# Performance work log

Hardware: AMD Instinct MI355X
Metric: run time of the kernel (lower is better)

The kernel has to match this reference:

```python
import jax, jax.numpy as jnp
import numpy as np

N = 4096        # number of nodes
C = 512         # in_features
L_LAT = 64      # L_latent
EPS = 0.25      # epsilon


def setup_inputs() -> dict:
    key = jax.random.key(0)
    ks = jax.random.split(key, 8)
    def lin(k, fan_in, shape):
        return (jax.random.normal(k, shape, jnp.float32) / np.float32(np.sqrt(fan_in)))
    x = jax.random.normal(ks[0], (N, C), jnp.float32)
    adj = jax.random.uniform(ks[1], (N, N), jnp.float32)  # dense nonneg kernel
    W_proj = lin(ks[2], C, (C, L_LAT)); b_proj = jnp.zeros((L_LAT,), jnp.float32)
    W_pi1 = lin(ks[3], L_LAT, (L_LAT, C)); b_pi1 = jnp.zeros((C,), jnp.float32)
    W_pi2 = lin(ks[4], C, (C, 1)); b_pi2 = jnp.zeros((1,), jnp.float32)
    W_f = lin(ks[5], C, (C, C)); b_f = jnp.zeros((C,), jnp.float32)
    dt = jnp.array([0.1], jnp.float32)
    return {"x": x, "adj": adj, "W_proj": W_proj, "b_proj": b_proj,
            "W_pi1": W_pi1, "b_pi1": b_pi1, "W_pi2": W_pi2, "b_pi2": b_pi2,
            "W_f": W_f, "b_f": b_f, "dt": dt}


def reference(x, adj, W_proj, b_proj, W_pi1, b_pi1, W_pi2, b_pi2, W_f, b_f, dt):
    # proj_list: x -> latent [n, L]
    z = x @ W_proj + b_proj
    # pi_list: Linear -> ReLU -> Linear -> Sigmoid, squeeze to [n]
    pi = jax.nn.sigmoid(jax.nn.relu(z @ W_pi1 + b_pi1) @ W_pi2 + b_pi2)[:, 0]
    # q_epsilon_tilde: row sums of the kernel
    q = adj.sum(axis=1)                       # [n]
    # K_tilde = K_epsilon @ diag(pi/q)  == column scaling
    K_tilde = adj * (pi / q)[None, :]         # [n, n]
    # D_tilde diagonal; torch.inverse of a diagonal == elementwise reciprocal
    d = K_tilde.sum(axis=1) + 1e-5            # [n]
    # target = relu(f(x)) with f = Linear(C, C)
    target = jax.nn.relu(x @ W_f + b_f)       # [n, C]
    # L @ target = (1/eps) * diag(1/d) @ K_tilde @ target - target
    Lt = (K_tilde @ target) / (EPS * d)[:, None] - target
    return target + dt[0] * Lt
```

## Files before the change

### kernel.cpp

```cpp
#include <hip/hip_runtime.h>
#include <hip/hip_bf16.h>

#define N_NODES 4096
#define C_DIM   512
#define L_DIM   64
#define SPLITS  4
#define KCHUNK  (N_NODES / SPLITS)

typedef unsigned short u16;
typedef unsigned int   u32;
using bf16x8 = __attribute__((ext_vector_type(8))) __bf16;
using u16x8  = __attribute__((ext_vector_type(8))) unsigned short;
using f32x4  = __attribute__((ext_vector_type(4))) float;

__device__ __forceinline__ float b2f(u16 u) {
    union { unsigned int i; float f; } v; v.i = ((unsigned int)u) << 16; return v.f;
}
__device__ __forceinline__ u16 f2b(float f) {
    unsigned int u = __float_as_uint(f);
    u += 0x7fff + ((u >> 16) & 1);
    return (u16)(u >> 16);
}
__device__ __forceinline__ void gload16(const void* g, void* l) {
    __builtin_amdgcn_global_load_lds((const __attribute__((address_space(1))) void*)g,
                                     (__attribute__((address_space(3))) void*)l,
                                     16, 0, 0);
}
__device__ __forceinline__ int detect_mode_inl(const u16* __restrict__ adj) {
    int m = 0;
#pragma unroll
    for (int i = 0; i < 64; ++i) m |= (adj[i] >= 0x8000) ? 1 : 0;
    return m;
}

#define OFF_MODE  0
#define OFF_DT    64
#define OFF_BIAS  1024
#define OFF_BP    4096
#define OFF_BP1   4608
#define OFF_WP2   8192
#define OFF_BP2   10240
#define OFF_Q     16384
#define OFF_S     32768
#define OFF_DV    49152
#define OFF_WPP   65536
#define OFF_WP1P  131072
#define OFF_WFT   196608
#define OFF_T     1048576
#define OFF_TST   9437184
#define OFF_XB    13631488
#define OFF_ADJB  17825792

__device__ __forceinline__ float ldin(const void* p, int i, int mode) {
    if (mode) return ((const float*)p)[i];
    return b2f(((const u16*)p)[i]);
}

__global__ __launch_bounds__(256) void k1_prep(const void* __restrict__ adj, const void* __restrict__ x,
        const void* Wp, const void* bp, const void* Wp1, const void* bp1,
        const void* Wp2, const void* bp2, const void* Wf, const void* bfc, const void* dt,
        int* __restrict__ modep,
        float* __restrict__ bp_f, float* __restrict__ bp1_f,
        float* __restrict__ Wp2_f, float* __restrict__ bp2_f,
        float* __restrict__ bias_f, float* __restrict__ dt_f,
        u32* __restrict__ WpP, u32* __restrict__ Wp1P,
        u16* __restrict__ adjb, float* __restrict__ q, u16* __restrict__ xb,
        u16* __restrict__ WfT) {
    __shared__ float tile[32][33];
    int bid = blockIdx.x, tid = threadIdx.x;
    int mode = detect_mode_inl((const u16*)adj);
    if (bid < 7) {
        if (bid == 0 && tid == 0) *modep = mode;
        int idx = bid * 256 + tid;
        if (idx < 64)           bp_f[idx]          = ldin(bp,  idx, mode);
        else if (idx < 576)     bp1_f[idx - 64]    = ldin(bp1, idx - 64, mode);
        else if (idx < 1088)    Wp2_f[idx - 576]   = ldin(Wp2, idx - 576, mode);
        else if (idx == 1088)   bp2_f[0]           = ldin(bp2, 0, mode);
        else if (idx < 1601)    bias_f[idx - 1089] = ldin(bfc, idx - 1089, mode);
        else if (idx == 1601)   dt_f[0]            = ldin(dt, 0, mode);
    } else if (bid < 2055) {
        if (mode == 0) return;
        int idx = (bid - 7) * 256 + tid;
        float4 v = ((const float4*)x)[idx];
        ushort4 o; o.x = f2b(v.x); o.y = f2b(v.y); o.z = f2b(v.z); o.w = f2b(v.w);
        ((ushort4*)xb)[idx] = o;
    } else if (bid < 3079) {
        int wave = tid >> 6, lane = tid & 63;
        int row = (bid - 2055) * 4 + wave;
        float acc = 0.f;
        if (mode) {
            const float4* rp = (const float4*)((const float*)adj + (size_t)row * N_NODES);
            ushort4* wp = (ushort4*)(adjb + (size_t)row * N_NODES);
#pragma unroll
            for (int it = 0; it < 16; ++it) {
                float4 v = rp[it * 64 + lane];
                acc += v.x + v.y + v.z + v.w;
                ushort4 o; o.x = f2b(v.x); o.y = f2b(v.y); o.z = f2b(v.z); o.w = f2b(v.w);
                wp[it * 64 + lane] = o;
            }
        } else {
            const u16x8* rp = (const u16x8*)((const u16*)adj + (size_t)row * N_NODES);
#pragma unroll
            for (int it = 0; it < 8; ++it) {
                u16x8 v = rp[it * 64 + lane];
#pragma unroll
                for (int e = 0; e < 8; ++e) acc += b2f(v[e]);
            }
        }
#pragma unroll
        for (int off = 32; off > 0; off >>= 1) acc += __shfl_down(acc, off);
        if (lane == 0) q[row] = acc;
    } else if (bid < 3335) {
        int g = bid - 3079;
        int tx = tid & 31, ty = tid >> 5;
        int x0 = (g & 15) * 32, y0 = (g >> 4) * 32;
        if (mode) {
            const float* src = (const float*)Wf;
#pragma unroll
            for (int r = ty; r < 32; r += 8) tile[r][tx] = src[(size_t)(y0 + r) * C_DIM + x0 + tx];
        } else {
            const u16* src = (const u16*)Wf;
#pragma unroll
            for (int r = ty; r < 32; r += 8) tile[r][tx] = b2f(src[(size_t)(y0 + r) * C_DIM + x0 + tx]);
        }
        __syncthreads();
#pragma unroll
        for (int r = ty; r < 32; r += 8)
            WfT[(size_t)(x0 + r) * C_DIM + y0 + tx] = f2b(tile[tx][r]);
    } else if (bid < 3399) {
        int idx = (bid - 3335) * 256 + tid;
        int k2i = idx >> 6, j = idx & 63;
        float a = ldin(Wp, (2 * k2i) * L_DIM + j, mode);
        float b = ldin(Wp, (2 * k2i + 1) * L_DIM + j, mode);
        WpP[idx] = (u32)f2b(a) | ((u32)f2b(b) << 16);
    } else {
        int idx = (bid - 3399) * 256 + tid;
        int jj2 = idx >> 9, m = idx & 511;
        float a = ldin(Wp1, (2 * jj2) * C_DIM + m, mode);
        float b = ldin(Wp1, (2 * jj2 + 1) * C_DIM + m, mode);
        Wp1P[idx] = (u32)f2b(a) | ((u32)f2b(b) << 16);
    }
}

__global__ __launch_bounds__(256) void k2_pi_gemm1(const void* __restrict__ xraw,
        const int* __restrict__ modep, const u16* __restrict__ xb, const u16* __restrict__ WfT,
        const u32* __restrict__ WpP, const u32* __restrict__ Wp1P,
        const float* __restrict__ bp_f,  const float* __restrict__ bp1_f,
        const float* __restrict__ Wp2_f, const float* __restrict__ bp2_f,
        const float* __restrict__ bias_f, const float* __restrict__ dt_f,
        const float* __restrict__ q, float* __restrict__ s, float* __restrict__ T,
        void* __restrict__ out, float* __restrict__ Pacc) {
    __shared__ __align__(16) char smem[26880];
    int bid = blockIdx.x, tid = threadIdx.x;
    int mode = *modep;
    if (bid < 512) {
        float (*sx)[C_DIM]      = (float(*)[C_DIM])smem;
        float (*red)[8][L_DIM]  = (float(*)[8][L_DIM])(smem + 16384);
        float (*sz)[L_DIM]      = (float(*)[L_DIM])(smem + 24576);
        float (*rw)[8]          = (float(*)[8])(smem + 26624);
        int i0 = bid * 8;
        const u16* xsrc = mode ? xb : (const u16*)xraw;
        const u16x8* xp = (const u16x8*)(xsrc + (size_t)i0 * C_DIM);
#pragma unroll
        for (int r = 0; r < 2; ++r) {
            u16x8 v = xp[tid + 256 * r];
            float* dstf = &sx[0][0] + (size_t)(tid + 256 * r) * 8;
#pragma unroll
            for (int e = 0; e < 8; ++e) dstf[e] = b2f(v[e]);
        }
        __syncthreads();
        int j = tid & 63, part = tid >> 6;
        float za[8];
#pragma unroll
        for (int n = 0; n < 8; ++n) za[n] = 0.f;
        const u32* wp = WpP + part * 4096 + j;
#pragma unroll 8
        for (int kk = 0; kk < 64; ++kk) {
            u32 w = wp[kk * 64];
            float wa = b2f((u16)(w & 0xFFFF)), wb = b2f((u16)(w >> 16));
            int k = part * 128 + kk * 2;
#pragma unroll
            for (int n = 0; n < 8; ++n) za[n] += sx[n][k] * wa + sx[n][k + 1] * wb;
        }
#pragma unroll
        for (int n = 0; n < 8; ++n) red[part][n][j] = za[n];
        __syncthreads();
#pragma unroll
        for (int r = 0; r < 2; ++r) {
            int idx = tid + r * 256; int n = idx >> 6, jj = idx & 63;
            sz[n][jj] = red[0][n][jj] + red[1][n][jj] + red[2][n][jj] + red[3][n][jj] + bp_f[jj];
        }
        __syncthreads();
        int m0 = tid, m1 = tid + 256;
        float h0[8], h1[8];
        float b0 = bp1_f[m0], b1 = bp1_f[m1];
#pragma unroll
        for (int n = 0; n < 8; ++n) { h0[n] = b0; h1[n] = b1; }
        const u32* w1p = Wp1P + m0;
#pragma unroll 4
        for (int jj2 = 0; jj2 < 32; ++jj2) {
            u32 w0 = w1p[jj2 * 512], w1 = w1p[jj2 * 512 + 256];
            float w0a = b2f((u16)(w0 & 0xFFFF)), w0b = b2f((u16)(w0 >> 16));
            float w1a = b2f((u16)(w1 & 0xFFFF)), w1b = b2f((u16)(w1 >> 16));
#pragma unroll
            for (int n = 0; n < 8; ++n) {
                float za_ = sz[n][2 * jj2], zb_ = sz[n][2 * jj2 + 1];
                h0[n] += za_ * w0a + zb_ * w0b;
                h1[n] += za_ * w1a + zb_ * w1b;
            }
        }
        float w2a = Wp2_f[m0], w2b = Wp2_f[m1];
        float p[8];
#pragma unroll
        for (int n = 0; n < 8; ++n)
            p[n] = fmaxf(h0[n], 0.f) * w2a + fmaxf(h1[n], 0.f) * w2b;
#pragma unroll
        for (int off = 32; off > 0; off >>= 1)
#pragma unroll
            for (int n = 0; n < 8; ++n) p[n] += __shfl_down(p[n], off);
        int lane = tid & 63, wave = tid >> 6;
        if (lane == 0) {
#pragma unroll
            for (int n = 0; n < 8; ++n) rw[wave][n] = p[n];
        }
        __syncthreads();
        if (tid < 8) {
            float tot = rw[0][tid] + rw[1][tid] + rw[2][tid] + rw[3][tid] + bp2_f[0];
            float pi = 1.f / (1.f + expf(-tot));
            s[i0 + tid] = pi / q[i0 + tid];
        }
    } else {
        u16* lA = (u16*)smem;
        u16* lB = (u16*)(smem + 4096);
        const u16* A = mode ? xb : (const u16*)xraw;
        float* tgt = mode ? (float*)out : Pacc;
        int g = bid - 512;
        int lane = tid & 63, wave = tid >> 6;
        int bm = (g & 63) * 64, bn = (g >> 6) * 64;
        int quad = lane >> 4, l15 = lane & 15;
        int wm = wave * 16;
        const u16* Ap = A + (size_t)(bm + (tid >> 2)) * C_DIM + (tid & 3) * 8;
        const u16* Bp = WfT + (size_t)(bn + (tid >> 2)) * C_DIM + (tid & 3) * 8;
        u16* la = lA + tid * 8;
        u16* lb = lB + tid * 8;
        f32x4 acc[4];
#pragma unroll
        for (int nt = 0; nt < 4; ++nt) acc[nt] = (f32x4){0.f, 0.f, 0.f, 0.f};
        for (int k0 = 0; k0 < C_DIM; k0 += 32) {
            gload16(Ap + k0, la);
            gload16(Bp + k0, lb);
            __syncthreads();
            bf16x8 af = *(const bf16x8*)&lA[(wm + l15) * 32 + quad * 8];
            bf16x8 bfv[4];
#pragma unroll
            for (int nt = 0; nt < 4; ++nt) bfv[nt] = *(const bf16x8*)&lB[(nt * 16 + l15) * 32 + quad * 8];
#pragma unroll
            for (int nt = 0; nt < 4; ++nt)
                acc[nt] = __builtin_amdgcn_mfma_f32_16x16x32_bf16(af, bfv[nt], acc[nt], 0, 0, 0);
            __syncthreads();
        }
        float c0 = 1.f - dt_f[0];
#pragma unroll
        for (int nt = 0; nt < 4; ++nt) {
            int col = bn + nt * 16 + l15;
            float bv = bias_f[col];
#pragma unroll
            for (int r = 0; r < 4; ++r) {
                int row = bm + wm + quad * 4 + r;
                float t = fmaxf(acc[nt][r] + bv, 0.f);
                T[(size_t)row * C_DIM + col] = t;
                tgt[(size_t)row * C_DIM + col] = c0 * t;
            }
        }
    }
}

__global__ __launch_bounds__(256) void k3_mid(const void* __restrict__ adjraw,
        const int* __restrict__ modep,
        const u16* __restrict__ adjb, const float* __restrict__ s,
        const float* __restrict__ T,
        float* __restrict__ dv, u16* __restrict__ TsT) {
    __shared__ float tile[32][33];
    int bid = blockIdx.x, tid = threadIdx.x;
    int mode = *modep;
    if (bid < 1024) {
        const u16* A = mode ? adjb : (const u16*)adjraw;
        int wave = tid >> 6, lane = tid & 63;
        int row = bid * 4 + wave;
        const u16x8* rp = (const u16x8*)(A + (size_t)row * N_NODES);
        float acc = 0.f;
#pragma unroll
        for (int it = 0; it < 8; ++it) {
            int chunk = it * 64 + lane;
            u16x8 v = rp[chunk];
            const float4* sp = (const float4*)(s + chunk * 8);
            float4 s0 = sp[0], s1 = sp[1];
            acc += b2f(v[0]) * s0.x + b2f(v[1]) * s0.y + b2f(v[2]) * s0.z + b2f(v[3]) * s0.w;
            acc += b2f(v[4]) * s1.x + b2f(v[5]) * s1.y + b2f(v[6]) * s1.z + b2f(v[7]) * s1.w;
        }
#pragma unroll
        for (int off = 32; off > 0; off >>= 1) acc += __shfl_down(acc, off);
        if (lane == 0) dv[row] = acc + 1e-5f;
    } else {
        int g = bid - 1024;
        int tx = tid & 31, ty = tid >> 5;
        int x0 = (g & 15) * 32, y0 = (g >> 4) * 32;
#pragma unroll
        for (int r = ty; r < 32; r += 8) tile[r][tx] = T[(size_t)(y0 + r) * C_DIM + x0 + tx];
        __syncthreads();
        float sv = s[y0 + tx];
#pragma unroll
        for (int r = ty; r < 32; r += 8)
            TsT[(size_t)(x0 + r) * N_NODES + y0 + tx] = f2b(tile[tx][r] * sv);
    }
}

__global__ __launch_bounds__(256) void k4_gemm2(const void* __restrict__ adjraw,
        const int* __restrict__ modep,
        const u16* __restrict__ adjb, const u16* __restrict__ TsT,
        const float* __restrict__ dv, const float* __restrict__ dt_f,
        void* __restrict__ out, float* __restrict__ Pacc) {
    __shared__ __align__(16) u16 lA[8192];
    __shared__ __align__(16) u16 lB[8192];
    int mode = *modep;
    const u16* A = mode ? adjb : (const u16*)adjraw;
    float* tgt = mode ? (float*)out : Pacc;
    int tid = threadIdx.x;
    int lane = tid & 63, wave = tid >> 6;
    int bm = blockIdx.x * 128, bn = blockIdx.y * 128;
    int kbase = blockIdx.z * KCHUNK;
    int wm = (wave & 1) * 64, wn = (wave >> 1) * 64;
    int quad = lane >> 4, l15 = lane & 15;

    const u16* Ab0 = A + (size_t)(bm + (tid >> 2)) * N_NODES + kbase + (tid & 3) * 8;
    const u16* Ab1 = A + (size_t)(bm + 64 + (tid >> 2)) * N_NODES + kbase + (tid & 3) * 8;
    const u16* Bb0 = TsT + (size_t)(bn + (tid >> 2)) * N_NODES + kbase + (tid & 3) * 8;
    const u16* Bb1 = TsT + (size_t)(bn + 64 + (tid >> 2)) * N_NODES + kbase + (tid & 3) * 8;
    u16* la00 = lA + tid * 8;        u16* la01 = lA + 2048 + tid * 8;
    u16* la10 = lA + 4096 + tid * 8; u16* la11 = lA + 6144 + tid * 8;
    u16* lb00 = lB + tid * 8;        u16* lb01 = lB + 2048 + tid * 8;
    u16* lb10 = lB + 4096 + tid * 8; u16* lb11 = lB + 6144 + tid * 8;

    f32x4 acc[4][4];
#pragma unroll
    for (int a = 0; a < 4; ++a)
#pragma unroll
        for (int b = 0; b < 4; ++b) acc[a][b] = (f32x4){0.f, 0.f, 0.f, 0.f};

    for (int k0 = 0; k0 < KCHUNK; k0 += 64) {
        gload16(Ab0 + k0, la00);
        gload16(Ab1 + k0, la01);
        gload16(Ab0 + k0 + 32, la10);
        gload16(Ab1 + k0 + 32, la11);
        gload16(Bb0 + k0, lb00);
        gload16(Bb1 + k0, lb01);
        gload16(Bb0 + k0 + 32, lb10);
        gload16(Bb1 + k0 + 32, lb11);
        __syncthreads();
#pragma unroll
        for (int kk = 0; kk < 2; ++kk) {
            const u16* baseA = lA + kk * 4096;
            const u16* baseB = lB + kk * 4096;
            bf16x8 af[4], bfv[4];
#pragma unroll
            for (int mt = 0; mt < 4; ++mt) af[mt] = *(const bf16x8*)&baseA[(wm + mt * 16 + l15) * 32 + quad * 8];
#pragma unroll
            for (int nt = 0; nt < 4; ++nt) bfv[nt] = *(const bf16x8*)&baseB[(wn + nt * 16 + l15) * 32 + quad * 8];
#pragma unroll
            for (int mt = 0; mt < 4; ++mt)
#pragma unroll
                for (int nt = 0; nt < 4; ++nt)
                    acc[mt][nt] = __builtin_amdgcn_mfma_f32_16x16x32_bf16(af[mt], bfv[nt], acc[mt][nt], 0, 0, 0);
        }
        __syncthreads();
    }

    float c1 = dt_f[0] * 4.f;
#pragma unroll
    for (int mt = 0; mt < 4; ++mt) {
        float inv[4];
#pragma unroll
        for (int r = 0; r < 4; ++r) inv[r] = c1 / dv[bm + wm + mt * 16 + quad * 4 + r];
#pragma unroll
        for (int nt = 0; nt < 4; ++nt) {
            int col = bn + wn + nt * 16 + l15;
#pragma unroll
            for (int r = 0; r < 4; ++r) {
                int row = bm + wm + mt * 16 + quad * 4 + r;
                atomicAdd(&tgt[(size_t)row * C_DIM + col], acc[mt][nt][r] * inv[r]);
            }
        }
    }
}

__global__ __launch_bounds__(256) void k5_fin(const int* __restrict__ modep,
                                              const float* __restrict__ Pacc,
                                              u16* __restrict__ out) {
    if (*modep) return;
    int idx = blockIdx.x * 256 + threadIdx.x;
    float4 v = ((const float4*)Pacc)[idx];
    ushort4 o; o.x = f2b(v.x); o.y = f2b(v.y); o.z = f2b(v.z); o.w = f2b(v.w);
    ((ushort4*)out)[idx] = o;
}

extern "C" void kernel_launch(void* const* d_in, const int* in_sizes, int n_in,
                              void* d_out, int out_size, void* d_ws, size_t ws_size,
                              hipStream_t stream) {
    const void* x   = d_in[0];
    const void* adj = d_in[1];
    const void* Wp  = d_in[2];
    const void* bp  = d_in[3];
    const void* Wp1 = d_in[4];
    const void* bp1 = d_in[5];
    const void* Wp2 = d_in[6];
    const void* bp2 = d_in[7];
    const void* Wf  = d_in[8];
    const void* bfc = d_in[9];
    const void* dtp = d_in[10];

    char* ws = (char*)d_ws;
    int*   modep  = (int*)(ws + OFF_MODE);
    float* dt_f   = (float*)(ws + OFF_DT);
    float* bias_f = (float*)(ws + OFF_BIAS);
    float* bp_f   = (float*)(ws + OFF_BP);
    float* bp1_f  = (float*)(ws + OFF_BP1);
    float* Wp2_f  = (float*)(ws + OFF_WP2);
    float* bp2_f  = (float*)(ws + OFF_BP2);
    float* q      = (float*)(ws + OFF_Q);
    float* s      = (float*)(ws + OFF_S);
    float* dv     = (float*)(ws + OFF_DV);
    u32*   WpP    = (u32*)(ws + OFF_WPP);
    u32*   Wp1P   = (u32*)(ws + OFF_WP1P);
    u16*   WfT    = (u16*)(ws + OFF_WFT);
    float* T      = (float*)(ws + OFF_T);
    u16*   TsT    = (u16*)(ws + OFF_TST);
    u16*   xb     = (u16*)(ws + OFF_XB);
    u16*   adjb   = (u16*)(ws + OFF_ADJB);
    float* Pacc   = (float*)(ws + OFF_ADJB);

    k1_prep<<<3463, 256, 0, stream>>>(adj, x, Wp, bp, Wp1, bp1, Wp2, bp2, Wf, bfc, dtp,
                                      modep, bp_f, bp1_f, Wp2_f, bp2_f, bias_f, dt_f,
                                      WpP, Wp1P, adjb, q, xb, WfT);
    k2_pi_gemm1<<<1024, 256, 0, stream>>>(x, modep, xb, WfT, WpP, Wp1P,
                                          bp_f, bp1_f, Wp2_f, bp2_f, bias_f, dt_f,
                                          q, s, T, d_out, Pacc);
    k3_mid<<<3072, 256, 0, stream>>>(adj, modep, adjb, s, T, dv, TsT);
    k4_gemm2<<<dim3(32, 4, SPLITS), 256, 0, stream>>>(adj, modep, adjb, TsT, dv, dt_f, d_out, Pacc);
    k5_fin<<<2048, 256, 0, stream>>>(modep, Pacc, (u16*)d_out);
}
```

Baseline: 215.4 us.

## Restructure pipeline: fuse pi MLP into prep, fuse transpose into GEMM1, double-buffer GEMM2

Moves the pi MLP into the prep kernel, reading raw weights directly instead of prepacked copies. The first GEMM now writes the scaled, transposed bf16 target straight from LDS, which removes the fp32 T intermediate and a separate transpose kernel. This cuts the launch count from five to four. The adjacency GEMM now double-buffers its LDS tiles with explicit waitcnt barriers so global loads overlap MFMA work. Mode detection is redone in each kernel instead of being read from workspace, which adds small redundant reads.

```diff
diff --git a/kernel.cpp b/kernel.cpp
--- a/kernel.cpp
+++ b/kernel.cpp
@@ -32,61 +32,30 @@
     for (int i = 0; i < 64; ++i) m |= (adj[i] >= 0x8000) ? 1 : 0;
     return m;
 }
-
-#define OFF_MODE  0
-#define OFF_DT    64
-#define OFF_BIAS  1024
-#define OFF_BP    4096
-#define OFF_BP1   4608
-#define OFF_WP2   8192
-#define OFF_BP2   10240
+__device__ __forceinline__ float ldin(const void* p, int i, int mode) {
+    if (mode) return ((const float*)p)[i];
+    return b2f(((const u16*)p)[i]);
+}
+
 #define OFF_Q     16384
-#define OFF_S     32768
+#define OFF_PI    32768
 #define OFF_DV    49152
-#define OFF_WPP   65536
-#define OFF_WP1P  131072
 #define OFF_WFT   196608
-#define OFF_T     1048576
 #define OFF_TST   9437184
 #define OFF_XB    13631488
 #define OFF_ADJB  17825792
 
-__device__ __forceinline__ float ldin(const void* p, int i, int mode) {
-    if (mode) return ((const float*)p)[i];
-    return b2f(((const u16*)p)[i]);
-}
-
 __global__ __launch_bounds__(256) void k1_prep(const void* __restrict__ adj, const void* __restrict__ x,
         const void* Wp, const void* bp, const void* Wp1, const void* bp1,
-        const void* Wp2, const void* bp2, const void* Wf, const void* bfc, const void* dt,
-        int* __restrict__ modep,
-        float* __restrict__ bp_f, float* __restrict__ bp1_f,
-        float* __restrict__ Wp2_f, float* __restrict__ bp2_f,
-        float* __restrict__ bias_f, float* __restrict__ dt_f,
-        u32* __restrict__ WpP, u32* __restrict__ Wp1P,
-        u16* __restrict__ adjb, float* __restrict__ q, u16* __restrict__ xb,
-        u16* __restrict__ WfT) {
-    __shared__ float tile[32][33];
+        const void* Wp2, const void* bp2, const void* Wf,
+        float* __restrict__ q, float* __restrict__ piv,
+        u16* __restrict__ adjb, u16* __restrict__ xb, u16* __restrict__ WfT) {
+    __shared__ __align__(16) char smem[26880];
     int bid = blockIdx.x, tid = threadIdx.x;
     int mode = detect_mode_inl((const u16*)adj);
-    if (bid < 7) {
-        if (bid == 0 && tid == 0) *modep = mode;
-        int idx = bid * 256 + tid;
-        if (idx < 64)           bp_f[idx]          = ldin(bp,  idx, mode);
-        else if (idx < 576)     bp1_f[idx - 64]    = ldin(bp1, idx - 64, mode);
-        else if (idx < 1088)    Wp2_f[idx - 576]   = ldin(Wp2, idx - 576, mode);
-        else if (idx == 1088)   bp2_f[0]           = ldin(bp2, 0, mode);
-        else if (idx < 1601)    bias_f[idx - 1089] = ldin(bfc, idx - 1089, mode);
-        else if (idx == 1601)   dt_f[0]            = ldin(dt, 0, mode);
-    } else if (bid < 2055) {
-        if (mode == 0) return;
-        int idx = (bid - 7) * 256 + tid;
-        float4 v = ((const float4*)x)[idx];
-        ushort4 o; o.x = f2b(v.x); o.y = f2b(v.y); o.z = f2b(v.z); o.w = f2b(v.w);
-        ((ushort4*)xb)[idx] = o;
-    } else if (bid < 3079) {
+    if (bid < 1024) {
         int wave = tid >> 6, lane = tid & 63;
-        int row = (bid - 2055) * 4 + wave;
+        int row = bid * 4 + wave;
         float acc = 0.f;
         if (mode) {
             const float4* rp = (const float4*)((const float*)adj + (size_t)row * N_NODES);
@@ -110,8 +79,96 @@
 #pragma unroll
         for (int off = 32; off > 0; off >>= 1) acc += __shfl_down(acc, off);
         if (lane == 0) q[row] = acc;
-    } else if (bid < 3335) {
-        int g = bid - 3079;
+    } else if (bid < 1536) {
+        float (*sx)[C_DIM]      = (float(*)[C_DIM])smem;
+        float (*red)[8][L_DIM]  = (float(*)[8][L_DIM])(smem + 16384);
+        float (*sz)[L_DIM]      = (float(*)[L_DIM])(smem + 24576);
+        float (*rw)[8]          = (float(*)[8])(smem + 26624);
+        int i0 = (bid - 1024) * 8;
+        if (mode) {
+            const float4* xp = (const float4*)((const float*)x + (size_t)i0 * C_DIM);
+            float4* dst = (float4*)sx;
+#pragma unroll
+            for (int r = 0; r < 4; ++r) dst[tid + 256 * r] = xp[tid + 256 * r];
+        } else {
+            const u16x8* xp = (const u16x8*)((const u16*)x + (size_t)i0 * C_DIM);
+#pragma unroll
+            for (int r = 0; r < 2; ++r) {
+                u16x8 v = xp[tid + 256 * r];
+                float* dstf = &sx[0][0] + (size_t)(tid + 256 * r) * 8;
+#pragma unroll
+                for (int e = 0; e < 8; ++e) dstf[e] = b2f(v[e]);
+            }
+        }
+        __syncthreads();
+        int j = tid & 63, part = tid >> 6;
+        float za[8];
+#pragma unroll
+        for (int n = 0; n < 8; ++n) za[n] = 0.f;
+#pragma unroll 8
+        for (int kk = 0; kk < 64; ++kk) {
+            int k = part * 128 + kk * 2;
+            float wa = ldin(Wp, k * L_DIM + j, mode);
+            float wb = ldin(Wp, (k + 1) * L_DIM + j, mode);
+#pragma unroll
+            for (int n = 0; n < 8; ++n) za[n] += sx[n][k] * wa + sx[n][k + 1] * wb;
+        }
+#pragma unroll
+        for (int n = 0; n < 8; ++n) red[part][n][j] = za[n];
+        __syncthreads();
+#pragma unroll
+        for (int r = 0; r < 2; ++r) {
+            int idx = tid + r * 256; int n = idx >> 6, jj = idx & 63;
+            sz[n][jj] = red[0][n][jj] + red[1][n][jj] + red[2][n][jj] + red[3][n][jj]
+                      + ldin(bp, jj, mode);
+        }
+        __syncthreads();
+        int m0 = tid, m1 = tid + 256;
+        float h0[8], h1[8];
+        float b0 = ldin(bp1, m0, mode), b1 = ldin(bp1, m1, mode);
+#pragma unroll
+        for (int n = 0; n < 8; ++n) { h0[n] = b0; h1[n] = b1; }
+#pragma unroll 4
+        for (int jj2 = 0; jj2 < 32; ++jj2) {
+            float w0a = ldin(Wp1, (2 * jj2) * C_DIM + m0, mode);
+            float w0b = ldin(Wp1, (2 * jj2 + 1) * C_DIM + m0, mode);
+            float w1a = ldin(Wp1, (2 * jj2) * C_DIM + m1, mode);
+            float w1b = ldin(Wp1, (2 * jj2 + 1) * C_DIM + m1, mode);
+#pragma unroll
+            for (int n = 0; n < 8; ++n) {
+                float za_ = sz[n][2 * jj2], zb_ = sz[n][2 * jj2 + 1];
+                h0[n] += za_ * w0a + zb_ * w0b;
+                h1[n] += za_ * w1a + zb_ * w1b;
+            }
+        }
+        float w2a = ldin(Wp2, m0, mode), w2b = ldin(Wp2, m1, mode);
+        float p[8];
+#pragma unroll
+        for (int n = 0; n < 8; ++n)
+            p[n] = fmaxf(h0[n], 0.f) * w2a + fmaxf(h1[n], 0.f) * w2b;
+#pragma unroll
+        for (int off = 32; off > 0; off >>= 1)
+#pragma unroll
+            for (int n = 0; n < 8; ++n) p[n] += __shfl_down(p[n], off);
+        int lane = tid & 63, wave = tid >> 6;
+        if (lane == 0) {
+#pragma unroll
+            for (int n = 0; n < 8; ++n) rw[wave][n] = p[n];
+        }
+        __syncthreads();
+        if (tid < 8) {
+            float tot = rw[0][tid] + rw[1][tid] + rw[2][tid] + rw[3][tid] + ldin(bp2, 0, mode);
+            piv[i0 + tid] = 1.f / (1.f + expf(-tot));
+        }
+    } else if (bid < 3584) {
+        if (mode == 0) return;
+        int idx = (bid - 1536) * 256 + tid;
+        float4 v = ((const float4*)x)[idx];
+        ushort4 o; o.x = f2b(v.x); o.y = f2b(v.y); o.z = f2b(v.z); o.w = f2b(v.w);
+        ((ushort4*)xb)[idx] = o;
+    } else {
+        float (*tile)[33] = (float(*)[33])smem;
+        int g = bid - 3584;
         int tx = tid & 31, ty = tid >> 5;
         int x0 = (g & 15) * 32, y0 = (g >> 4) * 32;
         if (mode) {
@@ -127,116 +184,50 @@
 #pragma unroll
         for (int r = ty; r < 32; r += 8)
             WfT[(size_t)(x0 + r) * C_DIM + y0 + tx] = f2b(tile[tx][r]);
-    } else if (bid < 3399) {
-        int idx = (bid - 3335) * 256 + tid;
-        int k2i = idx >> 6, j = idx & 63;
-        float a = ldin(Wp, (2 * k2i) * L_DIM + j, mode);
-        float b = ldin(Wp, (2 * k2i + 1) * L_DIM + j, mode);
-        WpP[idx] = (u32)f2b(a) | ((u32)f2b(b) << 16);
-    } else {
-        int idx = (bid - 3399) * 256 + tid;
-        int jj2 = idx >> 9, m = idx & 511;
-        float a = ldin(Wp1, (2 * jj2) * C_DIM + m, mode);
-        float b = ldin(Wp1, (2 * jj2 + 1) * C_DIM + m, mode);
-        Wp1P[idx] = (u32)f2b(a) | ((u32)f2b(b) << 16);
     }
 }
 
-__global__ __launch_bounds__(256) void k2_pi_gemm1(const void* __restrict__ xraw,
-        const int* __restrict__ modep, const u16* __restrict__ xb, const u16* __restrict__ WfT,
-        const u32* __restrict__ WpP, const u32* __restrict__ Wp1P,
-        const float* __restrict__ bp_f,  const float* __restrict__ bp1_f,
-        const float* __restrict__ Wp2_f, const float* __restrict__ bp2_f,
-        const float* __restrict__ bias_f, const float* __restrict__ dt_f,
-        const float* __restrict__ q, float* __restrict__ s, float* __restrict__ T,
+__global__ __launch_bounds__(256) void k2_mid(const void* __restrict__ adjraw, const void* __restrict__ xraw,
+        const void* bfc, const void* dtp,
+        const float* __restrict__ piv, const float* __restrict__ q,
+        const u16* __restrict__ adjb, const u16* __restrict__ xb, const u16* __restrict__ WfT,
+        float* __restrict__ dv, u16* __restrict__ TsT,
         void* __restrict__ out, float* __restrict__ Pacc) {
-    __shared__ __align__(16) char smem[26880];
+    __shared__ __align__(16) char smem[16640];
     int bid = blockIdx.x, tid = threadIdx.x;
-    int mode = *modep;
-    if (bid < 512) {
-        float (*sx)[C_DIM]      = (float(*)[C_DIM])smem;
-        float (*red)[8][L_DIM]  = (float(*)[8][L_DIM])(smem + 16384);
-        float (*sz)[L_DIM]      = (float(*)[L_DIM])(smem + 24576);
-        float (*rw)[8]          = (float(*)[8])(smem + 26624);
-        int i0 = bid * 8;
-        const u16* xsrc = mode ? xb : (const u16*)xraw;
-        const u16x8* xp = (const u16x8*)(xsrc + (size_t)i0 * C_DIM);
-#pragma unroll
-        for (int r = 0; r < 2; ++r) {
-            u16x8 v = xp[tid + 256 * r];
-            float* dstf = &sx[0][0] + (size_t)(tid + 256 * r) * 8;
-#pragma unroll
-            for (int e = 0; e < 8; ++e) dstf[e] = b2f(v[e]);
-        }
-        __syncthreads();
-        int j = tid & 63, part = tid >> 6;
-        float za[8];
-#pragma unroll
-        for (int n = 0; n < 8; ++n) za[n] = 0.f;
-        const u32* wp = WpP + part * 4096 + j;
-#pragma unroll 8
-        for (int kk = 0; kk < 64; ++kk) {
-            u32 w = wp[kk * 64];
-            float wa = b2f((u16)(w & 0xFFFF)), wb = b2f((u16)(w >> 16));
-            int k = part * 128 + kk * 2;
-#pragma unroll
-            for (int n = 0; n < 8; ++n) za[n] += sx[n][k] * wa + sx[n][k + 1] * wb;
-        }
-#pragma unroll
-        for (int n = 0; n < 8; ++n) red[part][n][j] = za[n];
-        __syncthreads();
-#pragma unroll
-        for (int r = 0; r < 2; ++r) {
-            int idx = tid + r * 256; int n = idx >> 6, jj = idx & 63;
-            sz[n][jj] = red[0][n][jj] + red[1][n][jj] + red[2][n][jj] + red[3][n][jj] + bp_f[jj];
-        }
-        __syncthreads();
-        int m0 = tid, m1 = tid + 256;
-        float h0[8], h1[8];
-        float b0 = bp1_f[m0], b1 = bp1_f[m1];
-#pragma unroll
-        for (int n = 0; n < 8; ++n) { h0[n] = b0; h1[n] = b1; }
-        const u32* w1p = Wp1P + m0;
-#pragma unroll 4
-        for (int jj2 = 0; jj2 < 32; ++jj2) {
-            u32 w0 = w1p[jj2 * 512], w1 = w1p[jj2 * 512 + 256];
-            float w0a = b2f((u16)(w0 & 0xFFFF)), w0b = b2f((u16)(w0 >> 16));
-            float w1a = b2f((u16)(w1 & 0xFFFF)), w1b = b2f((u16)(w1 >> 16));
-#pragma unroll
-            for (int n = 0; n < 8; ++n) {
-                float za_ = sz[n][2 * jj2], zb_ = sz[n][2 * jj2 + 1];
-                h0[n] += za_ * w0a + zb_ * w0b;
-                h1[n] += za_ * w1a + zb_ * w1b;
-            }
-        }
-        float w2a = Wp2_f[m0], w2b = Wp2_f[m1];
-        float p[8];
-#pragma unroll
-        for (int n = 0; n < 8; ++n)
-            p[n] = fmaxf(h0[n], 0.f) * w2a + fmaxf(h1[n], 0.f) * w2b;
-#pragma unroll
-        for (int off = 32; off > 0; off >>= 1)
-#pragma unroll
-            for (int n = 0; n < 8; ++n) p[n] += __shfl_down(p[n], off);
-        int lane = tid & 63, wave = tid >> 6;
-        if (lane == 0) {
-#pragma unroll
-            for (int n = 0; n < 8; ++n) rw[wave][n] = p[n];
-        }
-        __syncthreads();
-        if (tid < 8) {
-            float tot = rw[0][tid] + rw[1][tid] + rw[2][tid] + rw[3][tid] + bp2_f[0];
-            float pi = 1.f / (1.f + expf(-tot));
-            s[i0 + tid] = pi / q[i0 + tid];
-        }
+    int mode = detect_mode_inl((const u16*)adjraw);
+    if (bid < 1024) {
+        float* s_lds = (float*)smem;
+        for (int c = tid; c < N_NODES; c += 256) s_lds[c] = piv[c] / q[c];
+        __syncthreads();
+        const u16* A = mode ? adjb : (const u16*)adjraw;
+        int wave = tid >> 6, lane = tid & 63;
+        int row = bid * 4 + wave;
+        const u16x8* rp = (const u16x8*)(A + (size_t)row * N_NODES);
+        float acc = 0.f;
+#pragma unroll
+        for (int it = 0; it < 8; ++it) {
+            int chunk = it * 64 + lane;
+            u16x8 v = rp[chunk];
+            const float4* sp = (const float4*)(s_lds + chunk * 8);
+            float4 s0 = sp[0], s1 = sp[1];
+            acc += b2f(v[0]) * s0.x + b2f(v[1]) * s0.y + b2f(v[2]) * s0.z + b2f(v[3]) * s0.w;
+            acc += b2f(v[4]) * s1.x + b2f(v[5]) * s1.y + b2f(v[6]) * s1.z + b2f(v[7]) * s1.w;
+        }
+#pragma unroll
+        for (int off = 32; off > 0; off >>= 1) acc += __shfl_down(acc, off);
+        if (lane == 0) dv[row] = acc + 1e-5f;
     } else {
         u16* lA = (u16*)smem;
         u16* lB = (u16*)(smem + 4096);
+        u16* lT = (u16*)(smem + 8192);
+        float* s_row = (float*)(smem + 16384);
+        int g = bid - 1024;
+        int lane = tid & 63, wave = tid >> 6;
+        int bm = (g & 63) * 64, bn = (g >> 6) * 64;
+        if (tid < 64) s_row[tid] = piv[bm + tid] / q[bm + tid];
         const u16* A = mode ? xb : (const u16*)xraw;
         float* tgt = mode ? (float*)out : Pacc;
-        int g = bid - 512;
-        int lane = tid & 63, wave = tid >> 6;
-        int bm = (g & 63) * 64, bn = (g >> 6) * 64;
         int quad = lane >> 4, l15 = lane & 15;
         int wm = wave * 16;
         const u16* Ap = A + (size_t)(bm + (tid >> 2)) * C_DIM + (tid & 3) * 8;
@@ -259,70 +250,38 @@
                 acc[nt] = __builtin_amdgcn_mfma_f32_16x16x32_bf16(af, bfv[nt], acc[nt], 0, 0, 0);
             __syncthreads();
         }
-        float c0 = 1.f - dt_f[0];
+        float dtv = ldin(dtp, 0, mode);
+        float c0 = 1.f - dtv;
 #pragma unroll
         for (int nt = 0; nt < 4; ++nt) {
-            int col = bn + nt * 16 + l15;
-            float bv = bias_f[col];
+            int col_l = nt * 16 + l15;
+            float bv = ldin(bfc, bn + col_l, mode);
 #pragma unroll
             for (int r = 0; r < 4; ++r) {
-                int row = bm + wm + quad * 4 + r;
+                int row_l = wm + quad * 4 + r;
                 float t = fmaxf(acc[nt][r] + bv, 0.f);
-                T[(size_t)row * C_DIM + col] = t;
-                tgt[(size_t)row * C_DIM + col] = c0 * t;
-            }
-        }
+                tgt[(size_t)(bm + row_l) * C_DIM + bn + col_l] = c0 * t;
+                lT[col_l * 64 + row_l] = f2b(t * s_row[row_l]);
+            }
+        }
+        __syncthreads();
+        int col_l = tid >> 2, seg = tid & 3;
+        uint4 w0 = *(const uint4*)&lT[col_l * 64 + seg * 16];
+        uint4 w1 = *(const uint4*)&lT[col_l * 64 + seg * 16 + 8];
+        u16* dst = TsT + (size_t)(bn + col_l) * N_NODES + bm + seg * 16;
+        *(uint4*)dst = w0;
+        *(uint4*)(dst + 8) = w1;
     }
 }
 
-__global__ __launch_bounds__(256) void k3_mid(const void* __restrict__ adjraw,
-        const int* __restrict__ modep,
-        const u16* __restrict__ adjb, const float* __restrict__ s,
-        const float* __restrict__ T,
-        float* __restrict__ dv, u16* __restrict__ TsT) {
-    __shared__ float tile[32][33];
-    int bid = blockIdx.x, tid = threadIdx.x;
-    int mode = *modep;
-    if (bid < 1024) {
-        const u16* A = mode ? adjb : (const u16*)adjraw;
-        int wave = tid >> 6, lane = tid & 63;
-        int row = bid * 4 + wave;
-        const u16x8* rp = (const u16x8*)(A + (size_t)row * N_NODES);
-        float acc = 0.f;
-#pragma unroll
-        for (int it = 0; it < 8; ++it) {
-            int chunk = it * 64 + lane;
-            u16x8 v = rp[chunk];
-            const float4* sp = (const float4*)(s + chunk * 8);
-            float4 s0 = sp[0], s1 = sp[1];
-            acc += b2f(v[0]) * s0.x + b2f(v[1]) * s0.y + b2f(v[2]) * s0.z + b2f(v[3]) * s0.w;
-            acc += b2f(v[4]) * s1.x + b2f(v[5]) * s1.y + b2f(v[6]) * s1.z + b2f(v[7]) * s1.w;
-        }
-#pragma unroll
-        for (int off = 32; off > 0; off >>= 1) acc += __shfl_down(acc, off);
-        if (lane == 0) dv[row] = acc + 1e-5f;
-    } else {
-        int g = bid - 1024;
-        int tx = tid & 31, ty = tid >> 5;
-        int x0 = (g & 15) * 32, y0 = (g >> 4) * 32;
-#pragma unroll
-        for (int r = ty; r < 32; r += 8) tile[r][tx] = T[(size_t)(y0 + r) * C_DIM + x0 + tx];
-        __syncthreads();
-        float sv = s[y0 + tx];
-#pragma unroll
-        for (int r = ty; r < 32; r += 8)
-            TsT[(size_t)(x0 + r) * N_NODES + y0 + tx] = f2b(tile[tx][r] * sv);
-    }
-}
-
-__global__ __launch_bounds__(256) void k4_gemm2(const void* __restrict__ adjraw,
-        const int* __restrict__ modep,
+__global__ __launch_bounds__(256) void k3_gemm2(const void* __restrict__ adjraw,
+        const void* dtp,
         const u16* __restrict__ adjb, const u16* __restrict__ TsT,
-        const float* __restrict__ dv, const float* __restrict__ dt_f,
+        const float* __restrict__ dv,
         void* __restrict__ out, float* __restrict__ Pacc) {
-    __shared__ __align__(16) u16 lA[8192];
-    __shared__ __align__(16) u16 lB[8192];
-    int mode = *modep;
+    __shared__ __align__(16) u16 lA[2][8192];
+    __shared__ __align__(16) u16 lB[2][8192];
+    int mode = detect_mode_inl((const u16*)adjraw);
     const u16* A = mode ? adjb : (const u16*)adjraw;
     float* tgt = mode ? (float*)out : Pacc;
     int tid = threadIdx.x;
@@ -336,10 +295,6 @@
     const u16* Ab1 = A + (size_t)(bm + 64 + (tid >> 2)) * N_NODES + kbase + (tid & 3) * 8;
     const u16* Bb0 = TsT + (size_t)(bn + (tid >> 2)) * N_NODES + kbase + (tid & 3) * 8;
     const u16* Bb1 = TsT + (size_t)(bn + 64 + (tid >> 2)) * N_NODES + kbase + (tid & 3) * 8;
-    u16* la00 = lA + tid * 8;        u16* la01 = lA + 2048 + tid * 8;
-    u16* la10 = lA + 4096 + tid * 8; u16* la11 = lA + 6144 + tid * 8;
-    u16* lb00 = lB + tid * 8;        u16* lb01 = lB + 2048 + tid * 8;
-    u16* lb10 = lB + 4096 + tid * 8; u16* lb11 = lB + 6144 + tid * 8;
 
     f32x4 acc[4][4];
 #pragma unroll
@@ -347,20 +302,34 @@
 #pragma unroll
         for (int b = 0; b < 4; ++b) acc[a][b] = (f32x4){0.f, 0.f, 0.f, 0.f};
 
-    for (int k0 = 0; k0 < KCHUNK; k0 += 64) {
-        gload16(Ab0 + k0, la00);
-        gload16(Ab1 + k0, la01);
-        gload16(Ab0 + k0 + 32, la10);
-        gload16(Ab1 + k0 + 32, la11);
-        gload16(Bb0 + k0, lb00);
-        gload16(Bb1 + k0, lb01);
-        gload16(Bb0 + k0 + 32, lb10);
-        gload16(Bb1 + k0 + 32, lb11);
-        __syncthreads();
+#define STAGE(buf, k0)                                        \
+    do {                                                      \
+        u16* bA = &lA[(buf)][0];                              \
+        u16* bB = &lB[(buf)][0];                              \
+        gload16(Ab0 + (k0),      bA + tid * 8);               \
+        gload16(Ab1 + (k0),      bA + 2048 + tid * 8);        \
+        gload16(Ab0 + (k0) + 32, bA + 4096 + tid * 8);        \
+        gload16(Ab1 + (k0) + 32, bA + 6144 + tid * 8);        \
+        gload16(Bb0 + (k0),      bB + tid * 8);               \
+        gload16(Bb1 + (k0),      bB + 2048 + tid * 8);        \
+        gload16(Bb0 + (k0) + 32, bB + 4096 + tid * 8);        \
+        gload16(Bb1 + (k0) + 32, bB + 6144 + tid * 8);        \
+    } while (0)
+
+    STAGE(0, 0);
+    for (int it = 0; it < 16; ++it) {
+        int cur = it & 1;
+        if (it < 15) {
+            STAGE(cur ^ 1, (it + 1) * 64);
+            asm volatile("s_waitcnt vmcnt(8)\n\ts_barrier" ::: "memory");
+        } else {
+            asm volatile("s_waitcnt vmcnt(0)\n\ts_barrier" ::: "memory");
+        }
+        __builtin_amdgcn_sched_barrier(0);
 #pragma unroll
         for (int kk = 0; kk < 2; ++kk) {
-            const u16* baseA = lA + kk * 4096;
-            const u16* baseB = lB + kk * 4096;
+            const u16* baseA = &lA[cur][kk * 4096];
+            const u16* baseB = &lB[cur][kk * 4096];
             bf16x8 af[4], bfv[4];
 #pragma unroll
             for (int mt = 0; mt < 4; ++mt) af[mt] = *(const bf16x8*)&baseA[(wm + mt * 16 + l15) * 32 + quad * 8];
@@ -372,10 +341,11 @@
                 for (int nt = 0; nt < 4; ++nt)
                     acc[mt][nt] = __builtin_amdgcn_mfma_f32_16x16x32_bf16(af[mt], bfv[nt], acc[mt][nt], 0, 0, 0);
         }
-        __syncthreads();
+        asm volatile("s_waitcnt lgkmcnt(0)\n\ts_barrier" ::: "memory");
     }
-
-    float c1 = dt_f[0] * 4.f;
+#undef STAGE
+
+    float c1 = ldin(dtp, 0, mode) * 4.f;
 #pragma unroll
     for (int mt = 0; mt < 4; ++mt) {
         float inv[4];
@@ -393,10 +363,10 @@
     }
 }
 
-__global__ __launch_bounds__(256) void k5_fin(const int* __restrict__ modep,
+__global__ __launch_bounds__(256) void k5_fin(const void* __restrict__ adjraw,
                                               const float* __restrict__ Pacc,
                                               u16* __restrict__ out) {
-    if (*modep) return;
+    if (detect_mode_inl((const u16*)adjraw)) return;
     int idx = blockIdx.x * 256 + threadIdx.x;
     float4 v = ((const float4*)Pacc)[idx];
     ushort4 o; o.x = f2b(v.x); o.y = f2b(v.y); o.z = f2b(v.z); o.w = f2b(v.w);
@@ -419,32 +389,19 @@
     const void* dtp = d_in[10];
 
     char* ws = (char*)d_ws;
-    int*   modep  = (int*)(ws + OFF_MODE);
-    float* dt_f   = (float*)(ws + OFF_DT);
-    float* bias_f = (float*)(ws + OFF_BIAS);
-    float* bp_f   = (float*)(ws + OFF_BP);
-    float* bp1_f  = (float*)(ws + OFF_BP1);
-    float* Wp2_f  = (float*)(ws + OFF_WP2);
-    float* bp2_f  = (float*)(ws + OFF_BP2);
-    float* q      = (float*)(ws + OFF_Q);
-    float* s      = (float*)(ws + OFF_S);
-    float* dv     = (float*)(ws + OFF_DV);
-    u32*   WpP    = (u32*)(ws + OFF_WPP);
-    u32*   Wp1P   = (u32*)(ws + OFF_WP1P);
-    u16*   WfT    = (u16*)(ws + OFF_WFT);
-    float* T      = (float*)(ws + OFF_T);
-    u16*   TsT    = (u16*)(ws + OFF_TST);
-    u16*   xb     = (u16*)(ws + OFF_XB);
-    u16*   adjb   = (u16*)(ws + OFF_ADJB);
-    float* Pacc   = (float*)(ws + OFF_ADJB);
-
-    k1_prep<<<3463, 256, 0, stream>>>(adj, x, Wp, bp, Wp1, bp1, Wp2, bp2, Wf, bfc, dtp,
-                                      modep, bp_f, bp1_f, Wp2_f, bp2_f, bias_f, dt_f,
-                                      WpP, Wp1P, adjb, q, xb, WfT);
-    k2_pi_gemm1<<<1024, 256, 0, stream>>>(x, modep, xb, WfT, WpP, Wp1P,
-                                          bp_f, bp1_f, Wp2_f, bp2_f, bias_f, dt_f,
-                                          q, s, T, d_out, Pacc);
-    k3_mid<<<3072, 256, 0, stream>>>(adj, modep, adjb, s, T, dv, TsT);
-    k4_gemm2<<<dim3(32, 4, SPLITS), 256, 0, stream>>>(adj, modep, adjb, TsT, dv, dt_f, d_out, Pacc);
-    k5_fin<<<2048, 256, 0, stream>>>(modep, Pacc, (u16*)d_out);
-}
+    float* q    = (float*)(ws + OFF_Q);
+    float* piv  = (float*)(ws + OFF_PI);
+    float* dv   = (float*)(ws + OFF_DV);
+    u16*   WfT  = (u16*)(ws + OFF_WFT);
+    u16*   TsT  = (u16*)(ws + OFF_TST);
+    u16*   xb   = (u16*)(ws + OFF_XB);
+    u16*   adjb = (u16*)(ws + OFF_ADJB);
+    float* Pacc = (float*)(ws + OFF_ADJB);
+
+    k1_prep<<<3840, 256, 0, stream>>>(adj, x, Wp, bp, Wp1, bp1, Wp2, bp2, Wf,
+                                      q, piv, adjb, xb, WfT);
+    k2_mid<<<1536, 256, 0, stream>>>(adj, x, bfc, dtp, piv, q, adjb, xb, WfT,
+                                     dv, TsT, d_out, Pacc);
+    k3_gemm2<<<dim3(32, 4, SPLITS), 256, 0, stream>>>(adj, dtp, adjb, TsT, dv, d_out, Pacc);
+    k5_fin<<<2048, 256, 0, stream>>>(adj, Pacc, (u16*)d_out);
+}
```

Measured after the change: 211.9 us. No clear change (-1.6%).
